# Optimization experiments

Hardware: AMD Instinct MI355X
Metric: run time of the kernel (lower is better)

The kernel has to match this reference:

```python
import jax, jax.numpy as jnp
import numpy as np

N, C, T, V = 128, 256, 64, 32
FILTERS = 256

def setup_inputs() -> dict:
    key = jax.random.key(0)
    k1, k2, k3 = jax.random.split(key, 3)
    x = jax.random.normal(k1, (N, C, T, V), dtype=jnp.float32)
    a = jax.random.uniform(k2, (N, T, V, V), dtype=jnp.float32)
    # 1x1 Conv2D (channels_first) == pointwise channel projection: weight [C_in, filters]
    W = jax.random.normal(k3, (C, FILTERS), dtype=jnp.float32) * (2.0 / FILTERS) ** 0.5
    b = jnp.zeros((FILTERS,), dtype=jnp.float32)
    return {"x": x, "a": a, "W": W, "b": b}

def reference(x, a, W, b):
    # 1x1 conv over channels_first input: [n,c,t,v] -> [n,f,t,v]
    h = jnp.einsum('nctv,cf->nftv', x, W) + b[None, :, None, None]
    # Dropout is identity at inference (training=False).
    # Per-frame graph convolution: contract vertex dim with adjacency.
    out = jnp.einsum('nctv,ntvw->nctw', h, a)
    return (out, a)
```

## Files before the change

### kernel.cpp

```cpp
#include <hip/hip_runtime.h>


#define NN 128
#define CC 256
#define TT 64
#define VV 32
#define FF 256
#define TB 2

typedef _Float16 half8 __attribute__((ext_vector_type(8)));
typedef _Float16 half4 __attribute__((ext_vector_type(4)));
typedef float floatx4 __attribute__((ext_vector_type(4)));

__global__ __launch_bounds__(256) void wt_prep_kernel(const float* __restrict__ W,
                                                      _Float16* __restrict__ Wt) {
    const int c = blockIdx.x;
    const int f = threadIdx.x;
    Wt[f * CC + c] = (_Float16)W[c * FF + f];
}

__global__ __launch_bounds__(256, 2) void sgcn_mfma13_kernel(
    const float* __restrict__ x, const float* __restrict__ a,
    const _Float16* __restrict__ Wt, const float* __restrict__ b,
    float* __restrict__ out, float* __restrict__ out_a)
{
    __shared__ _Float16 a_t[TB * VV * VV];
    __shared__ _Float16 g_s[TB * VV * 256];
    __shared__ float    s_lds[TB][VV];

    const int tid  = threadIdx.x;
    const int lane = tid & 63;
    const int wv   = tid >> 6;
    const int l15  = lane & 15;
    const int lg   = lane >> 4;
    const int blk  = blockIdx.x;
    const int n    = blk >> 5;
    const int t0   = (blk & 31) * TB;

    char* at_base = (char*)a_t;
    char* g_base  = (char*)g_s;

    const int tA    = wv >> 1;
    const int chalf = wv & 1;

    float4 xf[16];
    #pragma unroll
    for (int ci = 0; ci < 8; ++ci) {
        const int c = (chalf * 8 + ci) * 16 + l15;
        const float* xp = x + (((size_t)n * CC + c) * TT + (t0 + tA)) * VV + 8 * lg;
        xf[ci * 2 + 0] = *reinterpret_cast<const float4*>(xp);
        xf[ci * 2 + 1] = *reinterpret_cast<const float4*>(xp + 4);
    }

    #pragma unroll
    for (int k = 0; k < 2; ++k) {
        const int o  = (tid + 256 * k) * 4;
        const int it = o >> 10;
        const int r  = o & 1023;
        const int v  = r >> 5;
        const int w0 = r & 31;
        const size_t off = ((size_t)(n * TT + t0 + it)) * (VV * VV) + r;
        float4 av = *reinterpret_cast<const float4*>(a + off);
        *reinterpret_cast<float4*>(out_a + off) = av;
        #pragma unroll
        for (int j = 0; j < 4; ++j) {
            const int row = it * VV + w0 + j;
            const float e = j == 0 ? av.x : j == 1 ? av.y : j == 2 ? av.z : av.w;
            *reinterpret_cast<_Float16*>(at_base + row * 64 +
                                         ((v * 2) ^ ((row & 3) << 4))) = (_Float16)e;
        }
    }

    __syncthreads();

    if (tid < TB * VV) {
        const int it = tid >> 5, w = tid & 31;
        const int row = it * VV + w;
        float ss = 0.0f;
        #pragma unroll
        for (int v = 0; v < VV; ++v)
            ss += (float)*reinterpret_cast<const _Float16*>(
                at_base + row * 64 + ((v * 2) ^ ((row & 3) << 4)));
        s_lds[it][w] = ss;
    }

    {
        const int ra = tA * VV + l15, rb = ra + 16;
        half8 bA0 = *reinterpret_cast<const half8*>(at_base + ra * 64 +
                                                    ((16 * lg) ^ ((ra & 3) << 4)));
        half8 bA1 = *reinterpret_cast<const half8*>(at_base + rb * 64 +
                                                    ((16 * lg) ^ ((rb & 3) << 4)));
        char* gt = g_base + tA * (VV * 256 * 2);
        #pragma unroll
        for (int ci = 0; ci < 8; ++ci) {
            const int ct = chalf * 8 + ci;
            half8 af;
            float4 x0 = xf[ci * 2 + 0], x1 = xf[ci * 2 + 1];
            af[0] = (_Float16)x0.x; af[1] = (_Float16)x0.y;
            af[2] = (_Float16)x0.z; af[3] = (_Float16)x0.w;
            af[4] = (_Float16)x1.x; af[5] = (_Float16)x1.y;
            af[6] = (_Float16)x1.z; af[7] = (_Float16)x1.w;
            #pragma unroll
            for (int wt = 0; wt < 2; ++wt) {
                floatx4 acc = {0.f, 0.f, 0.f, 0.f};
                acc = __builtin_amdgcn_mfma_f32_16x16x32_f16(af, wt ? bA1 : bA0, acc, 0, 0, 0);
                half4 gh;
                gh[0] = (_Float16)acc[0]; gh[1] = (_Float16)acc[1];
                gh[2] = (_Float16)acc[2]; gh[3] = (_Float16)acc[3];
                const int row = 16 * wt + l15;
                const int cb  = (ct * 16 + 4 * lg) * 2;
                *reinterpret_cast<half4*>(gt + row * 512 + (cb ^ ((row & 7) << 4))) = gh;
            }
        }
    }

    __syncthreads();

    #pragma unroll
    for (int fth = 0; fth < 4; ++fth) {
        const int ft = wv * 4 + fth;
        const int f  = ft * 16 + l15;
        half8 wb[8];
        const _Float16* wp = Wt + (size_t)f * CC + 8 * lg;
        #pragma unroll
        for (int ks = 0; ks < 8; ++ks)
            wb[ks] = *reinterpret_cast<const half8*>(wp + 32 * ks);
        const float bvf = b[f];

        #pragma unroll
        for (int tt = 0; tt < TB; ++tt) {
            char* gt = g_base + tt * (VV * 256 * 2);
            floatx4 acc2[2];
            acc2[0] = (floatx4){0.f, 0.f, 0.f, 0.f};
            acc2[1] = (floatx4){0.f, 0.f, 0.f, 0.f};

            __builtin_amdgcn_s_setprio(1);
            #pragma unroll
            for (int ks = 0; ks < 8; ++ks) {
                const int rr0 = l15, rr1 = 16 + l15;
                const int cb = (32 * ks + 8 * lg) * 2;
                half8 ga0 = *reinterpret_cast<const half8*>(gt + rr0 * 512 +
                                                            (cb ^ ((rr0 & 7) << 4)));
                half8 ga1 = *reinterpret_cast<const half8*>(gt + rr1 * 512 +
                                                            (cb ^ ((rr1 & 7) << 4)));
                acc2[0] = __builtin_amdgcn_mfma_f32_16x16x32_f16(ga0, wb[ks], acc2[0], 0, 0, 0);
                acc2[1] = __builtin_amdgcn_mfma_f32_16x16x32_f16(ga1, wb[ks], acc2[1], 0, 0, 0);
            }
            __builtin_amdgcn_s_setprio(0);

            float* ob = out + (((size_t)n * FF + f) * TT + (t0 + tt)) * VV;
            #pragma unroll
            for (int mt = 0; mt < 2; ++mt) {
                const int w0 = 16 * mt + 4 * lg;
                float4 sv = *reinterpret_cast<const float4*>(&s_lds[tt][w0]);
                float4 o;
                o.x = acc2[mt][0] + bvf * sv.x;
                o.y = acc2[mt][1] + bvf * sv.y;
                o.z = acc2[mt][2] + bvf * sv.z;
                o.w = acc2[mt][3] + bvf * sv.w;
                *reinterpret_cast<float4*>(ob + w0) = o;
            }
        }
    }
}

__global__ __launch_bounds__(256) void sgcn_fused_kernel(
    const float* __restrict__ x, const float* __restrict__ a,
    const float* __restrict__ W, const float* __restrict__ b,
    float* __restrict__ out, float* __restrict__ out_a)
{
    __shared__ float x_lds[CC][VV];
    __shared__ float a_lds[VV][VV];
    const int tid = threadIdx.x;
    const int nt  = blockIdx.x;
    const int n   = nt >> 6;
    const int t   = nt & 63;
    const float* xb = x + (size_t)n * CC * TT * VV + (size_t)t * VV;
    #pragma unroll
    for (int k = 0; k < 8; ++k) {
        int e = tid * 4 + k * 1024;
        int c = e >> 5, v = e & 31;
        float4 val = *reinterpret_cast<const float4*>(xb + (size_t)c * (TT * VV) + v);
        *reinterpret_cast<float4*>(&x_lds[c][v]) = val;
    }
    {
        const float* ab = a + (size_t)nt * (VV * VV);
        float4 av = *reinterpret_cast<const float4*>(ab + tid * 4);
        *reinterpret_cast<float4*>(&a_lds[0][0] + tid * 4) = av;
        *reinterpret_cast<float4*>(out_a + (size_t)nt * (VV * VV) + tid * 4) = av;
    }
    __syncthreads();
    const int f = tid;
    float h[VV];
    #pragma unroll
    for (int v = 0; v < VV; ++v) h[v] = 0.0f;
    #pragma unroll 4
    for (int c = 0; c < CC; ++c) {
        float wv = W[c * FF + f];
        #pragma unroll
        for (int v = 0; v < VV; ++v) h[v] = fmaf(x_lds[c][v], wv, h[v]);
    }
    const float bias = b[f];
    #pragma unroll
    for (int v = 0; v < VV; ++v) h[v] += bias;
    float o[VV];
    #pragma unroll
    for (int w = 0; w < VV; ++w) o[w] = 0.0f;
    #pragma unroll
    for (int v = 0; v < VV; ++v) {
        float hv = h[v];
        #pragma unroll
        for (int w = 0; w < VV; ++w) o[w] = fmaf(hv, a_lds[v][w], o[w]);
    }
    float* ob = out + (((size_t)n * FF + f) * TT + t) * VV;
    #pragma unroll
    for (int w = 0; w < VV; w += 4)
        *reinterpret_cast<float4*>(ob + w) = make_float4(o[w], o[w+1], o[w+2], o[w+3]);
}

extern "C" void kernel_launch(void* const* d_in, const int* in_sizes, int n_in,
                              void* d_out, int out_size, void* d_ws, size_t ws_size,
                              hipStream_t stream) {
    const float* x = (const float*)d_in[0];
    const float* a = (const float*)d_in[1];
    const float* W = (const float*)d_in[2];
    const float* b = (const float*)d_in[3];

    float* out   = (float*)d_out;
    float* out_a = out + (size_t)NN * FF * TT * VV;

    const size_t wt_bytes = (size_t)FF * CC * sizeof(_Float16);

    if (ws_size >= wt_bytes) {
        _Float16* Wt = (_Float16*)d_ws;
        wt_prep_kernel<<<dim3(CC), dim3(FF), 0, stream>>>(W, Wt);
        sgcn_mfma13_kernel<<<dim3(NN * (TT / TB)), dim3(256), 0, stream>>>(x, a, Wt, b, out, out_a);
    } else {
        sgcn_fused_kernel<<<dim3(NN * TT), dim3(256), 0, stream>>>(x, a, W, b, out, out_a);
    }
}
```

Before: 178.4 us.

## Double frames per block, load adjacency fragments directly from global, drop LDS staging

Each block now processes four frames with 512 threads instead of two frames with 256, so each wave covers fewer filter tiles and each W fragment load feeds more MFMA work. The adjacency matrix is no longer transposed through LDS. Each wave gathers its MFMA B fragments and the row sums straight from global memory with strided scalar loads, which removes one barrier and the a_t buffer. The setprio hints are also removed. The gathers are uncoalesced, and the larger LDS footprint and block size may reduce occupancy.

```diff
diff --git a/kernel.cpp b/kernel.cpp
--- a/kernel.cpp
+++ b/kernel.cpp
@@ -6,7 +6,7 @@
 #define TT 64
 #define VV 32
 #define FF 256
-#define TB 2
+#define TB 4
 
 typedef _Float16 half8 __attribute__((ext_vector_type(8)));
 typedef _Float16 half4 __attribute__((ext_vector_type(4)));
@@ -19,12 +19,11 @@
     Wt[f * CC + c] = (_Float16)W[c * FF + f];
 }
 
-__global__ __launch_bounds__(256, 2) void sgcn_mfma13_kernel(
+__global__ __launch_bounds__(512, 2) void sgcn_mfma14_kernel(
     const float* __restrict__ x, const float* __restrict__ a,
     const _Float16* __restrict__ Wt, const float* __restrict__ b,
     float* __restrict__ out, float* __restrict__ out_a)
 {
-    __shared__ _Float16 a_t[TB * VV * VV];
     __shared__ _Float16 g_s[TB * VV * 256];
     __shared__ float    s_lds[TB][VV];
 
@@ -34,14 +33,15 @@
     const int l15  = lane & 15;
     const int lg   = lane >> 4;
     const int blk  = blockIdx.x;
-    const int n    = blk >> 5;
-    const int t0   = (blk & 31) * TB;
-
-    char* at_base = (char*)a_t;
-    char* g_base  = (char*)g_s;
+    const int n    = blk >> 4;
+    const int t0   = (blk & 15) * TB;
+
+    char* g_base = (char*)g_s;
 
     const int tA    = wv >> 1;
     const int chalf = wv & 1;
+
+    const float* a_blk = a + ((size_t)(n * TT + t0)) * (VV * VV);
 
     float4 xf[16];
     #pragma unroll
@@ -52,44 +52,34 @@
         xf[ci * 2 + 1] = *reinterpret_cast<const float4*>(xp + 4);
     }
 
+    half8 bA0, bA1;
+    {
+        const float* at = a_blk + (size_t)tA * (VV * VV);
+        #pragma unroll
+        for (int j = 0; j < 8; ++j) {
+            const float* row = at + (8 * lg + j) * VV;
+            bA0[j] = (_Float16)row[l15];
+            bA1[j] = (_Float16)row[16 + l15];
+        }
+    }
+
     #pragma unroll
     for (int k = 0; k < 2; ++k) {
-        const int o  = (tid + 256 * k) * 4;
-        const int it = o >> 10;
-        const int r  = o & 1023;
-        const int v  = r >> 5;
-        const int w0 = r & 31;
-        const size_t off = ((size_t)(n * TT + t0 + it)) * (VV * VV) + r;
-        float4 av = *reinterpret_cast<const float4*>(a + off);
-        *reinterpret_cast<float4*>(out_a + off) = av;
-        #pragma unroll
-        for (int j = 0; j < 4; ++j) {
-            const int row = it * VV + w0 + j;
-            const float e = j == 0 ? av.x : j == 1 ? av.y : j == 2 ? av.z : av.w;
-            *reinterpret_cast<_Float16*>(at_base + row * 64 +
-                                         ((v * 2) ^ ((row & 3) << 4))) = (_Float16)e;
-        }
-    }
-
-    __syncthreads();
+        const int o = (tid + 512 * k) * 4;
+        float4 av = *reinterpret_cast<const float4*>(a_blk + o);
+        *reinterpret_cast<float4*>(out_a + ((size_t)(n * TT + t0)) * (VV * VV) + o) = av;
+    }
 
     if (tid < TB * VV) {
         const int it = tid >> 5, w = tid & 31;
-        const int row = it * VV + w;
+        const float* at = a_blk + (size_t)it * (VV * VV) + w;
         float ss = 0.0f;
         #pragma unroll
-        for (int v = 0; v < VV; ++v)
-            ss += (float)*reinterpret_cast<const _Float16*>(
-                at_base + row * 64 + ((v * 2) ^ ((row & 3) << 4)));
+        for (int v = 0; v < VV; ++v) ss += at[v * VV];
         s_lds[it][w] = ss;
     }
 
     {
-        const int ra = tA * VV + l15, rb = ra + 16;
-        half8 bA0 = *reinterpret_cast<const half8*>(at_base + ra * 64 +
-                                                    ((16 * lg) ^ ((ra & 3) << 4)));
-        half8 bA1 = *reinterpret_cast<const half8*>(at_base + rb * 64 +
-                                                    ((16 * lg) ^ ((rb & 3) << 4)));
         char* gt = g_base + tA * (VV * 256 * 2);
         #pragma unroll
         for (int ci = 0; ci < 8; ++ci) {
@@ -117,8 +107,8 @@
     __syncthreads();
 
     #pragma unroll
-    for (int fth = 0; fth < 4; ++fth) {
-        const int ft = wv * 4 + fth;
+    for (int fth = 0; fth < 2; ++fth) {
+        const int ft = fth * 8 + wv;
         const int f  = ft * 16 + l15;
         half8 wb[8];
         const _Float16* wp = Wt + (size_t)f * CC + 8 * lg;
@@ -134,7 +124,6 @@
             acc2[0] = (floatx4){0.f, 0.f, 0.f, 0.f};
             acc2[1] = (floatx4){0.f, 0.f, 0.f, 0.f};
 
-            __builtin_amdgcn_s_setprio(1);
             #pragma unroll
             for (int ks = 0; ks < 8; ++ks) {
                 const int rr0 = l15, rr1 = 16 + l15;
@@ -146,7 +135,6 @@
                 acc2[0] = __builtin_amdgcn_mfma_f32_16x16x32_f16(ga0, wb[ks], acc2[0], 0, 0, 0);
                 acc2[1] = __builtin_amdgcn_mfma_f32_16x16x32_f16(ga1, wb[ks], acc2[1], 0, 0, 0);
             }
-            __builtin_amdgcn_s_setprio(0);
 
             float* ob = out + (((size_t)n * FF + f) * TT + (t0 + tt)) * VV;
             #pragma unroll
@@ -234,7 +222,7 @@
     if (ws_size >= wt_bytes) {
         _Float16* Wt = (_Float16*)d_ws;
         wt_prep_kernel<<<dim3(CC), dim3(FF), 0, stream>>>(W, Wt);
-        sgcn_mfma13_kernel<<<dim3(NN * (TT / TB)), dim3(256), 0, stream>>>(x, a, Wt, b, out, out_a);
+        sgcn_mfma14_kernel<<<dim3(NN * (TT / TB)), dim3(512), 0, stream>>>(x, a, Wt, b, out, out_a);
     } else {
         sgcn_fused_kernel<<<dim3(NN * TT), dim3(256), 0, stream>>>(x, a, W, b, out, out_a);
     }
```

Measured after the change: 150.4 us. 15.7% less time.
